# Performance work log

Measured on AMD Instinct MI355X. Metric: run time of the kernel, lower is better.

Reference implementation:

```python
import jax, jax.numpy as jnp
import numpy as np

RADIUS = 7
EPS = 0.01
K = 2 * RADIUS + 1  # 15x15 box kernel
# TF tf.image.rgb_to_grayscale luma weights
RGB_W = np.array([0.2989, 0.5870, 0.1140], dtype=np.float32)


def setup_inputs() -> dict:
    key = jax.random.key(0)
    # images in [-1, 1], NHWC
    x = jax.random.uniform(key, (16, 512, 512, 3), jnp.float32, -1.0, 1.0)
    return {"x": x}


def reference(x):
    inputs = (x + 1.0) * 0.5  # map to [0, 1]
    # grayscale guidance: [B, H, W, 1]
    guidance = jnp.einsum('bhwc,c->bhw', inputs, jnp.asarray(RGB_W, dtype=x.dtype))[..., None]
    guidance = guidance - jnp.mean(guidance) + jnp.mean(inputs)
    # 15x15 uniform box blur (depthwise conv on the single guidance channel), SAME zero padding
    kernel = jnp.full((K, K, 1, 1), 1.0 / (K * K), dtype=x.dtype)  # HWIO
    smoothed = jax.lax.conv_general_dilated(
        guidance, kernel, window_strides=(1, 1), padding='SAME',
        dimension_numbers=('NHWC', 'HWIO', 'NHWC'))
    out = inputs * (1.0 - EPS) + smoothed * EPS  # smoothed broadcasts over 3 channels
    return out * 2.0 - 1.0
```

## Files before the change

### kernel.cpp

```cpp
#include <hip/hip_runtime.h>


#define BATCH  16
#define HEIGHT 512
#define WIDTH  512
#define NPIX   (BATCH * HEIGHT * WIDTH)
#define RAD    7
#define KS     15
#define EPSV   0.01f

#define W_R 0.2989f
#define W_G 0.5870f
#define W_B 0.1140f

__global__ __launch_bounds__(256) void k_luma_hblur(const float* __restrict__ x,
                                                    float* __restrict__ tmp,
                                                    float2* __restrict__ partials) {
    __shared__ float sx[3072];
    __shared__ float sl[2][528];
    __shared__ float redG[4], redI[4];
    int t = threadIdx.x;

    if (t < 7) {
        sl[0][t] = 0.f; sl[1][t] = 0.f;
        sl[0][519 + t] = 0.f; sl[1][519 + t] = 0.f;
    }

    size_t base4 = (size_t)blockIdx.x * 768;
    const float4* xv = (const float4*)x;
    float4* s4 = (float4*)sx;
#pragma unroll
    for (int i = 0; i < 3; i++)
        s4[i * 256 + t] = xv[base4 + i * 256 + t];
    __syncthreads();

    float sG = 0.f, sI = 0.f;
#pragma unroll
    for (int i = 0; i < 4; i++) {
        int p  = t + (i << 8);
        int lr = p >> 9;
        int c  = p & (WIDTH - 1);
        float r  = (sx[3 * p + 0] + 1.f) * 0.5f;
        float gg = (sx[3 * p + 1] + 1.f) * 0.5f;
        float bb = (sx[3 * p + 2] + 1.f) * 0.5f;
        float l  = W_R * r + W_G * gg + W_B * bb;
        sl[lr][RAD + c] = l;
        sG += l;
        sI += r + gg + bb;
    }

#pragma unroll
    for (int off = 32; off > 0; off >>= 1) {
        sG += __shfl_down(sG, off, 64);
        sI += __shfl_down(sI, off, 64);
    }
    int lane = t & 63, wave = t >> 6;
    if (lane == 0) { redG[wave] = sG; redI[wave] = sI; }
    __syncthreads();

    if (t == 0)
        partials[blockIdx.x] = make_float2(redG[0] + redG[1] + redG[2] + redG[3],
                                           redI[0] + redI[1] + redI[2] + redI[3]);

    int row_g = blockIdx.x * 2;
#pragma unroll
    for (int i = 0; i < 4; i++) {
        int p  = t + (i << 8);
        int lr = p >> 9;
        int c  = p & (WIDTH - 1);
        float sum = 0.f;
#pragma unroll
        for (int d = 0; d < KS; d++) sum += sl[lr][c + d];
        tmp[(size_t)(row_g + lr) * WIDTH + c] = sum;
    }
}

__global__ __launch_bounds__(256) void k_reduce(const float2* __restrict__ partials,
                                                float* __restrict__ sums) {
    int t = threadIdx.x;
    float sG = 0.f, sI = 0.f;
    for (int i = t; i < 4096; i += 256) {
        float2 v = partials[i];
        sG += v.x; sI += v.y;
    }
#pragma unroll
    for (int off = 32; off > 0; off >>= 1) {
        sG += __shfl_down(sG, off, 64);
        sI += __shfl_down(sI, off, 64);
    }
    __shared__ float rG[4], rI[4];
    int lane = t & 63, wave = t >> 6;
    if (lane == 0) { rG[wave] = sG; rI[wave] = sI; }
    __syncthreads();
    if (t == 0) {
        float SG = rG[0] + rG[1] + rG[2] + rG[3];
        float SI = rI[0] + rI[1] + rI[2] + rI[3];
        float meanG = SG * (1.f / (float)NPIX);
        float meanI = SI * (1.f / (3.f * (float)NPIX));
        sums[0] = meanI - meanG;
    }
}

__global__ __launch_bounds__(256) void k_vblur_combine(const float* __restrict__ tmp,
                                                       const float* __restrict__ x,
                                                       float* __restrict__ out,
                                                       const float* __restrict__ sums) {
    __shared__ float sAdd[1024];
    int t = threadIdx.x;
    int R = blockIdx.x * 2;
    int b = R >> 9;
    int y = R & (HEIGHT - 1);
    int lr  = t >> 7;
    int col = (t << 2) & (WIDTH - 1);
    int yy0 = y + lr;
    float offset = sums[0];

    const float* base = tmp + ((size_t)b * HEIGHT) * WIDTH + col;
    float s0 = 0.f, s1 = 0.f, s2 = 0.f, s3 = 0.f;
#pragma unroll
    for (int d = -RAD; d <= RAD; d++) {
        int yy = yy0 + d;
        if (yy >= 0 && yy < HEIGHT) {
            float4 v = *(const float4*)(base + (size_t)yy * WIDTH);
            s0 += v.x; s1 += v.y; s2 += v.z; s3 += v.w;
        }
    }
    const float nrm = 1.f / (float)(KS * KS);
    float cy = (float)(min(yy0, RAD) + 1 + min(HEIGHT - 1 - yy0, RAD));
    float c0 = (float)(min(col + 0, RAD) + 1 + min(WIDTH - 1 - col, RAD));
    float c1 = (float)(min(col + 1, RAD) + 1 + min(WIDTH - 2 - col, RAD));
    float c2 = (float)(min(col + 2, RAD) + 1 + min(WIDTH - 3 - col, RAD));
    float c3 = (float)(min(col + 3, RAD) + 1 + min(WIDTH - 4 - col, RAD));
    int lp = t << 2;
    sAdd[lp + 0] = EPSV * (2.f * (s0 + offset * c0 * cy) * nrm - 1.f);
    sAdd[lp + 1] = EPSV * (2.f * (s1 + offset * c1 * cy) * nrm - 1.f);
    sAdd[lp + 2] = EPSV * (2.f * (s2 + offset * c2 * cy) * nrm - 1.f);
    sAdd[lp + 3] = EPSV * (2.f * (s3 + offset * c3 * cy) * nrm - 1.f);
    __syncthreads();

    const float scale = 1.f - EPSV;
    size_t base4 = (size_t)blockIdx.x * 768;
    const float4* xv = (const float4*)x;
    float4*       ov = (float4*)out;
#pragma unroll
    for (int i = 0; i < 3; i++) {
        int q = i * 256 + t;
        float4 xi = xv[base4 + q];
        float4 o;
        o.x = xi.x * scale + sAdd[(4 * q + 0) / 3];
        o.y = xi.y * scale + sAdd[(4 * q + 1) / 3];
        o.z = xi.z * scale + sAdd[(4 * q + 2) / 3];
        o.w = xi.w * scale + sAdd[(4 * q + 3) / 3];
        ov[base4 + q] = o;
    }
}

extern "C" void kernel_launch(void* const* d_in, const int* in_sizes, int n_in,
                              void* d_out, int out_size, void* d_ws, size_t ws_size,
                              hipStream_t stream) {
    const float* x   = (const float*)d_in[0];
    float*       out = (float*)d_out;

    float*  sums     = (float*)d_ws;
    float2* partials = (float2*)((char*)d_ws + 256);
    float*  tmp      = (float*)((char*)d_ws + 256 + 4096 * sizeof(float2));

    const int NBLK = BATCH * HEIGHT / 2;

    k_luma_hblur<<<NBLK, 256, 0, stream>>>(x, tmp, partials);
    k_reduce<<<1, 256, 0, stream>>>(partials, sums);
    k_vblur_combine<<<NBLK, 256, 0, stream>>>(tmp, x, out, sums);
}
```

Baseline: 128.1 us.

## Use running-sum vertical blur over 16-row bands in combine kernel

The vertical blur/combine kernel now processes a 16-row band per 128-thread block and keeps a sliding vertical sum per column (add the incoming row, subtract the outgoing one). This replaces 15 loads per output row with about 2, and removes the shared-memory staging and barrier. In exchange there are far fewer blocks (512 of 128 threads), which cuts parallelism and latency hiding, and each thread's global accesses are now 3 strided float4s per row.

Measured after the change: 119.1 us. 1.08x faster.

```diff
diff --git a/kernel.cpp b/kernel.cpp
--- a/kernel.cpp
+++ b/kernel.cpp
@@ -101,57 +101,70 @@
     }
 }
 
-__global__ __launch_bounds__(256) void k_vblur_combine(const float* __restrict__ tmp,
+#define TROWS 16
+__global__ __launch_bounds__(128) void k_vblur_combine(const float* __restrict__ tmp,
                                                        const float* __restrict__ x,
                                                        float* __restrict__ out,
                                                        const float* __restrict__ sums) {
-    __shared__ float sAdd[1024];
-    int t = threadIdx.x;
-    int R = blockIdx.x * 2;
-    int b = R >> 9;
-    int y = R & (HEIGHT - 1);
-    int lr  = t >> 7;
-    int col = (t << 2) & (WIDTH - 1);
-    int yy0 = y + lr;
+    int t    = threadIdx.x;
+    int band = blockIdx.x & (HEIGHT / TROWS - 1);
+    int b    = blockIdx.x >> 5;
+    int y0   = band * TROWS;
     float offset = sums[0];
+    const float nrm   = 1.f / (float)(KS * KS);
+    const float scale = 1.f - EPSV;
 
-    const float* base = tmp + ((size_t)b * HEIGHT) * WIDTH + col;
-    float s0 = 0.f, s1 = 0.f, s2 = 0.f, s3 = 0.f;
-#pragma unroll
-    for (int d = -RAD; d <= RAD; d++) {
-        int yy = yy0 + d;
-        if (yy >= 0 && yy < HEIGHT) {
-            float4 v = *(const float4*)(base + (size_t)yy * WIDTH);
-            s0 += v.x; s1 += v.y; s2 += v.z; s3 += v.w;
-        }
-    }
-    const float nrm = 1.f / (float)(KS * KS);
-    float cy = (float)(min(yy0, RAD) + 1 + min(HEIGHT - 1 - yy0, RAD));
+    int col = t << 2;
     float c0 = (float)(min(col + 0, RAD) + 1 + min(WIDTH - 1 - col, RAD));
     float c1 = (float)(min(col + 1, RAD) + 1 + min(WIDTH - 2 - col, RAD));
     float c2 = (float)(min(col + 2, RAD) + 1 + min(WIDTH - 3 - col, RAD));
     float c3 = (float)(min(col + 3, RAD) + 1 + min(WIDTH - 4 - col, RAD));
-    int lp = t << 2;
-    sAdd[lp + 0] = EPSV * (2.f * (s0 + offset * c0 * cy) * nrm - 1.f);
-    sAdd[lp + 1] = EPSV * (2.f * (s1 + offset * c1 * cy) * nrm - 1.f);
-    sAdd[lp + 2] = EPSV * (2.f * (s2 + offset * c2 * cy) * nrm - 1.f);
-    sAdd[lp + 3] = EPSV * (2.f * (s3 + offset * c3 * cy) * nrm - 1.f);
-    __syncthreads();
 
-    const float scale = 1.f - EPSV;
-    size_t base4 = (size_t)blockIdx.x * 768;
-    const float4* xv = (const float4*)x;
-    float4*       ov = (float4*)out;
+    const float4* tv = (const float4*)tmp + (size_t)b * HEIGHT * (WIDTH / 4) + t;
+
+    float s0 = 0.f, s1 = 0.f, s2 = 0.f, s3 = 0.f;
+    int rlo = y0 - RAD < 0 ? 0 : y0 - RAD;
+    for (int r = rlo; r <= y0 + RAD; ++r) {
+        float4 v = tv[(size_t)r * (WIDTH / 4)];
+        s0 += v.x; s1 += v.y; s2 += v.z; s3 += v.w;
+    }
+
+    const float4* xv = (const float4*)x   + (size_t)b * HEIGHT * 384;
+    float4*       ov = (float4*)out       + (size_t)b * HEIGHT * 384;
+
 #pragma unroll
-    for (int i = 0; i < 3; i++) {
-        int q = i * 256 + t;
-        float4 xi = xv[base4 + q];
-        float4 o;
-        o.x = xi.x * scale + sAdd[(4 * q + 0) / 3];
-        o.y = xi.y * scale + sAdd[(4 * q + 1) / 3];
-        o.z = xi.z * scale + sAdd[(4 * q + 2) / 3];
-        o.w = xi.w * scale + sAdd[(4 * q + 3) / 3];
-        ov[base4 + q] = o;
+    for (int i = 0; i < TROWS; ++i) {
+        int y = y0 + i;
+        float cy = (float)(min(y, RAD) + 1 + min(HEIGHT - 1 - y, RAD));
+        float k  = offset * cy;
+        float a0 = EPSV * (2.f * (s0 + k * c0) * nrm - 1.f);
+        float a1 = EPSV * (2.f * (s1 + k * c1) * nrm - 1.f);
+        float a2 = EPSV * (2.f * (s2 + k * c2) * nrm - 1.f);
+        float a3 = EPSV * (2.f * (s3 + k * c3) * nrm - 1.f);
+
+        size_t rb = (size_t)y * 384 + 3 * t;
+        float4 x0 = xv[rb + 0];
+        float4 x1 = xv[rb + 1];
+        float4 x2 = xv[rb + 2];
+        float4 o0, o1, o2;
+        o0.x = x0.x * scale + a0; o0.y = x0.y * scale + a0;
+        o0.z = x0.z * scale + a0; o0.w = x0.w * scale + a1;
+        o1.x = x1.x * scale + a1; o1.y = x1.y * scale + a1;
+        o1.z = x1.z * scale + a2; o1.w = x1.w * scale + a2;
+        o2.x = x2.x * scale + a2; o2.y = x2.y * scale + a3;
+        o2.z = x2.z * scale + a3; o2.w = x2.w * scale + a3;
+        ov[rb + 0] = o0;
+        ov[rb + 1] = o1;
+        ov[rb + 2] = o2;
+
+        if (y + RAD + 1 < HEIGHT) {
+            float4 v = tv[(size_t)(y + RAD + 1) * (WIDTH / 4)];
+            s0 += v.x; s1 += v.y; s2 += v.z; s3 += v.w;
+        }
+        if (y - RAD >= 0) {
+            float4 v = tv[(size_t)(y - RAD) * (WIDTH / 4)];
+            s0 -= v.x; s1 -= v.y; s2 -= v.z; s3 -= v.w;
+        }
     }
 }
 
@@ -165,9 +178,7 @@
     float2* partials = (float2*)((char*)d_ws + 256);
     float*  tmp      = (float*)((char*)d_ws + 256 + 4096 * sizeof(float2));
 
-    const int NBLK = BATCH * HEIGHT / 2;
-
-    k_luma_hblur<<<NBLK, 256, 0, stream>>>(x, tmp, partials);
+    k_luma_hblur<<<BATCH * HEIGHT / 2, 256, 0, stream>>>(x, tmp, partials);
     k_reduce<<<1, 256, 0, stream>>>(partials, sums);
-    k_vblur_combine<<<NBLK, 256, 0, stream>>>(tmp, x, out, sums);
+    k_vblur_combine<<<BATCH * (HEIGHT / TROWS), 128, 0, stream>>>(tmp, x, out, sums);
 }
```
